# Performance work log

Hardware: AMD Instinct MI355X
Metric: run time of the kernel (lower is better)

The kernel has to match this reference:

```python
import jax, jax.numpy as jnp
import numpy as np
from itertools import combinations_with_replacement

LATENT_DIM = 16
N_PARAMS = 2
N_VARS = LATENT_DIM + N_PARAMS  # 18
POLY_ORDER = 3
BATCH = 131072

# Static exponent index tables: for each degree d, an [n_terms_d, d] array of
# variable indices (combinations with replacement), matching a sympy-style
# polynomial library [1, x_i, x_i*x_j, x_i*x_j*x_k, ...].
IDX = [np.array(list(combinations_with_replacement(range(N_VARS), d)), dtype=np.int32)
       for d in range(1, POLY_ORDER + 1)]
P = 1 + sum(a.shape[0] for a in IDX)  # 1330 library terms


def setup_inputs() -> dict:
    key = jax.random.key(0)
    k1, k2, k3 = jax.random.split(key, 3)
    z = jax.random.normal(k1, (BATCH, LATENT_DIM), dtype=jnp.float32)
    betas = jax.random.normal(k2, (BATCH, N_PARAMS), dtype=jnp.float32)
    big_xi = jax.random.normal(k3, (P, N_VARS), dtype=jnp.float32) * 0.1
    mask = jnp.ones((P, N_VARS), dtype=jnp.float32)
    return {"z": z, "betas": betas, "big_xi": big_xi, "mask": mask}


def _theta(x):
    # x: [B, N_VARS] -> theta: [B, P]
    cols = [jnp.ones((x.shape[0], 1), dtype=x.dtype)]  # constant term
    for idx in IDX:
        acc = x[:, idx[:, 0]]                # [B, n_terms_d]
        for k in range(1, idx.shape[1]):     # loop over degree (<= POLY_ORDER)
            acc = acc * x[:, idx[:, k]]
        cols.append(acc)
    return jnp.concatenate(cols, axis=1)


def reference(z, betas, big_xi, mask):
    x = jnp.concatenate([z, betas], axis=1)  # [B, N_VARS]
    theta = _theta(x)                        # [B, P]
    return theta @ (big_xi * mask)           # [B, N_VARS]
```

## Files before the change

kernel.cpp:

```cpp
#include <hip/hip_runtime.h>
#include <hip/hip_bf16.h>
#include <utility>


constexpr int NVARS   = 18;
constexpr int NOUT    = 18;
constexpr int NROWS   = 131072;
constexpr int PTERMS  = 1330;
constexpr int NSLOTS  = 672;
constexpr int NREPS   = 670;
constexpr int NCHUNKS = 84;

typedef __attribute__((ext_vector_type(8)))  short short8;
typedef __attribute__((ext_vector_type(16))) float f32x16;

struct T3 { int a, b, c; };

constexpr int sig(int v) { return v < 18 ? (v + 9) % 18 : v; }

constexpr T3 sigma3(T3 t) {
    int u0 = sig(t.a), u1 = sig(t.b), u2 = sig(t.c);
    int tmp = 0;
    if (u0 > u1) { tmp = u0; u0 = u1; u1 = tmp; }
    if (u1 > u2) { tmp = u1; u1 = u2; u2 = tmp; }
    if (u0 > u1) { tmp = u0; u0 = u1; u1 = tmp; }
    return T3{u0, u1, u2};
}

constexpr bool t3_less(T3 x, T3 y) {
    if (x.a != y.a) return x.a < y.a;
    if (x.b != y.b) return x.b < y.b;
    return x.c < y.c;
}
constexpr bool t3_eq(T3 x, T3 y) { return x.a == y.a && x.b == y.b && x.c == y.c; }

constexpr int rank_of(T3 t) {
    int deg = (t.a < 18) + (t.b < 18) + (t.c < 18);
    if (deg == 0) return 0;
    if (deg == 1) return 1 + t.a;
    if (deg == 2) {
        int r = 19;
        for (int a = 0; a < t.a; ++a) r += 18 - a;
        return r + (t.b - t.a);
    }
    int r = 190;
    for (int a = 0; a < t.a; ++a) { int n = 18 - a; r += n * (n + 1) / 2; }
    for (int b = t.a; b < t.b; ++b) r += 18 - b;
    return r + (t.c - t.b);
}

struct RepTables {
    signed char va[NSLOTS], vb[NSLOTS], vc[NSLOTS];
    short p0[NSLOTS], p1[NSLOTS];
};

constexpr RepTables make_tables() {
    RepTables R{};
    int s = 0;
    {
        T3 t{18, 18, 18};
        R.va[s] = 18; R.vb[s] = 18; R.vc[s] = 18;
        R.p0[s] = 0; R.p1[s] = -1;
        ++s;
    }
    for (int a = 0; a < NVARS; ++a) {
        T3 t{a, 18, 18};
        T3 st = sigma3(t);
        if (!t3_less(st, t)) {
            R.va[s] = (signed char)a; R.vb[s] = 18; R.vc[s] = 18;
            R.p0[s] = (short)rank_of(t);
            R.p1[s] = t3_eq(st, t) ? (short)-1 : (short)rank_of(st);
            ++s;
        }
    }
    for (int a = 0; a < NVARS; ++a)
        for (int b = a; b < NVARS; ++b) {
            T3 t{a, b, 18};
            T3 st = sigma3(t);
            if (!t3_less(st, t)) {
                R.va[s] = (signed char)a; R.vb[s] = (signed char)b; R.vc[s] = 18;
                R.p0[s] = (short)rank_of(t);
                R.p1[s] = t3_eq(st, t) ? (short)-1 : (short)rank_of(st);
                ++s;
            }
        }
    for (int a = 0; a < NVARS; ++a)
        for (int b = a; b < NVARS; ++b)
            for (int c = b; c < NVARS; ++c) {
                T3 t{a, b, c};
                T3 st = sigma3(t);
                if (!t3_less(st, t)) {
                    R.va[s] = (signed char)a; R.vb[s] = (signed char)b; R.vc[s] = (signed char)c;
                    R.p0[s] = (short)rank_of(t);
                    R.p1[s] = t3_eq(st, t) ? (short)-1 : (short)rank_of(st);
                    ++s;
                }
            }
    for (; s < NSLOTS; ++s) {
        R.va[s] = 19; R.vb[s] = 19; R.vc[s] = 19;
        R.p0[s] = -1; R.p1[s] = -1;
    }
    return R;
}

constexpr RepTables h_tab = make_tables();
__device__ const RepTables d_tab = make_tables();


__device__ __forceinline__ unsigned pack2(float f0, float f1) {
    unsigned u0 = __float_as_uint(f0) + 0x8000u;
    unsigned u1 = __float_as_uint(f1) + 0x8000u;
    return __builtin_amdgcn_perm(u1, u0, 0x07060302u);
}

template <int S>
__device__ __forceinline__ float term_val(const float (&x)[NVARS]) {
    constexpr int a = h_tab.va[S], b = h_tab.vb[S], c = h_tab.vc[S];
    if constexpr (a >= 19)      return 0.0f;
    else if constexpr (a == 18) return 1.0f;
    else if constexpr (b == 18) return x[a];
    else if constexpr (c == 18) return x[a] * x[b];
    else                        return x[a] * x[b] * x[c];
}

union AFrag { unsigned u[4]; short8 v; };

template <int CI, int... I>
__device__ __forceinline__ void eval8(const float (&x)[NVARS], float (&t)[8],
                                      std::integer_sequence<int, I...>) {
    ((t[I] = term_val<CI * 8 + I>(x)), ...);
}

template <int CI>
__device__ __forceinline__ void kstep(const float (&x)[NVARS],
                                      const short* __restrict__ wlane, f32x16& acc) {
    float t[8];
    eval8<CI>(x, t, std::make_integer_sequence<int, 8>{});
    AFrag af;
#pragma unroll
    for (int j = 0; j < 4; ++j) af.u[j] = pack2(t[2 * j], t[2 * j + 1]);
    short8 bf = *(const short8*)(wlane + CI * 512);
    acc = __builtin_amdgcn_mfma_f32_32x32x16_bf16(af.v, bf, acc, 0, 0, 0);
}

template <int... CI>
__device__ __forceinline__ void kloop(const float (&x)[NVARS],
                                      const short* __restrict__ wlane, f32x16& acc,
                                      std::integer_sequence<int, CI...>) {
    (kstep<CI>(x, wlane, acc), ...);
}

__global__ __launch_bounds__(256, 4) void vindy_mfma(const float* __restrict__ z,
                                                     const float* __restrict__ betas,
                                                     const short* __restrict__ wf,
                                                     float* __restrict__ out) {
    const int lane = threadIdx.x & 63;
    const int wave = threadIdx.x >> 6;
    const int m    = lane & 31;
    const int half = lane >> 5;
    const int row  = blockIdx.x * 128 + wave * 32 + m;

    float xr[NVARS];
    {
        const float4* z4 = (const float4*)(z + (size_t)row * 16);
        float4 v0 = z4[0], v1 = z4[1], v2 = z4[2], v3 = z4[3];
        xr[0]  = v0.x; xr[1]  = v0.y; xr[2]  = v0.z; xr[3]  = v0.w;
        xr[4]  = v1.x; xr[5]  = v1.y; xr[6]  = v1.z; xr[7]  = v1.w;
        xr[8]  = v2.x; xr[9]  = v2.y; xr[10] = v2.z; xr[11] = v2.w;
        xr[12] = v3.x; xr[13] = v3.y; xr[14] = v3.z; xr[15] = v3.w;
        const float2 b2 = *(const float2*)(betas + (size_t)row * 2);
        xr[16] = b2.x; xr[17] = b2.y;
    }
    const bool hp = (half != 0);
    float x[NVARS];
#pragma unroll
    for (int v = 0; v < NVARS; ++v) x[v] = hp ? xr[(v + 9) % NVARS] : xr[v];

    f32x16 acc;
#pragma unroll
    for (int i = 0; i < 16; ++i) acc[i] = 0.0f;

    const short* wlane = wf + lane * 8;
    kloop(x, wlane, acc, std::make_integer_sequence<int, NCHUNKS>{});

    if (m < NOUT) {
        float* op = out + ((size_t)(blockIdx.x * 128 + wave * 32 + half * 4)) * NOUT + m;
#pragma unroll
        for (int r = 0; r < 16; ++r) {
            int rr = (r & 3) + 8 * (r >> 2);
            op[(size_t)rr * NOUT] = acc[r];
        }
    }
}


__global__ void prep_wfrag(const float* __restrict__ xi, const float* __restrict__ mask,
                           __hip_bfloat16* __restrict__ wf) {
    int i = blockIdx.x * blockDim.x + threadIdx.x;
    if (i >= NCHUNKS * 64 * 8) return;
    int j = i & 7;
    int l = (i >> 3) & 63;
    int c = i >> 9;
    int s = c * 8 + j;
    int n = l & 31;
    int h = l >> 5;
    int p = h ? (int)d_tab.p1[s] : (int)d_tab.p0[s];
    float v = 0.0f;
    if (p >= 0 && n < NOUT) v = xi[p * NOUT + n] * mask[p * NOUT + n];
    wf[i] = __float2bfloat16(v);
}

extern "C" void kernel_launch(void* const* d_in, const int* in_sizes, int n_in,
                              void* d_out, int out_size, void* d_ws, size_t ws_size,
                              hipStream_t stream) {
    const float* z     = (const float*)d_in[0];
    const float* betas = (const float*)d_in[1];
    const float* xi    = (const float*)d_in[2];
    const float* mask  = (const float*)d_in[3];
    __hip_bfloat16* wf = (__hip_bfloat16*)d_ws;
    float* out = (float*)d_out;

    const int nprep = NCHUNKS * 64 * 8;
    prep_wfrag<<<(nprep + 255) / 256, 256, 0, stream>>>(xi, mask, wf);
    vindy_mfma<<<NROWS / 128, 256, 0, stream>>>(z, betas, (const short*)d_ws, out);
}
```

Before: 94.92 us.

## Use order-4 variable symmetry orbits with 16x16x32 MFMA to halve term evaluation

```diff
diff --git a/kernel.cpp b/kernel.cpp
--- a/kernel.cpp
+++ b/kernel.cpp
@@ -7,25 +7,30 @@
 constexpr int NOUT    = 18;
 constexpr int NROWS   = 131072;
 constexpr int PTERMS  = 1330;
-constexpr int NSLOTS  = 672;
-constexpr int NREPS   = 670;
-constexpr int NCHUNKS = 84;
-
-typedef __attribute__((ext_vector_type(8)))  short short8;
-typedef __attribute__((ext_vector_type(16))) float f32x16;
+constexpr int NCHUNKS = 43;
+constexpr int NSLOTS  = NCHUNKS * 8;
+
+typedef __attribute__((ext_vector_type(8))) short short8;
+typedef __attribute__((ext_vector_type(4))) float f32x4;
 
 struct T3 { int a, b, c; };
 
-constexpr int sig(int v) { return v < 18 ? (v + 9) % 18 : v; }
-
-constexpr T3 sigma3(T3 t) {
-    int u0 = sig(t.a), u1 = sig(t.b), u2 = sig(t.c);
-    int tmp = 0;
-    if (u0 > u1) { tmp = u0; u0 = u1; u1 = tmp; }
-    if (u1 > u2) { tmp = u1; u1 = u2; u2 = tmp; }
-    if (u0 > u1) { tmp = u0; u0 = u1; u1 = tmp; }
+constexpr int rho1(int v) {
+    if (v < 16)  return (v & ~3) | ((v + 1) & 3);
+    if (v == 16) return 17;
+    if (v == 17) return 16;
+    return v;
+}
+constexpr int rho2v(int v) { return rho1(rho1(v)); }
+
+constexpr T3 sort3(int u0, int u1, int u2) {
+    int t = 0;
+    if (u0 > u1) { t = u0; u0 = u1; u1 = t; }
+    if (u1 > u2) { t = u1; u1 = u2; u2 = t; }
+    if (u0 > u1) { t = u0; u0 = u1; u1 = t; }
     return T3{u0, u1, u2};
 }
+constexpr T3 rho3(T3 t) { return sort3(rho1(t.a), rho1(t.b), rho1(t.c)); }
 
 constexpr bool t3_less(T3 x, T3 y) {
     if (x.a != y.a) return x.a < y.a;
@@ -51,67 +56,64 @@
 
 struct RepTables {
     signed char va[NSLOTS], vb[NSLOTS], vc[NSLOTS];
-    short p0[NSLOTS], p1[NSLOTS];
+    short p[4][NSLOTS];
+    int count;
 };
+
+constexpr void consider(RepTables& R, int& s, T3 t) {
+    T3 im[4] = {t, T3{0, 0, 0}, T3{0, 0, 0}, T3{0, 0, 0}};
+    im[1] = rho3(im[0]);
+    im[2] = rho3(im[1]);
+    im[3] = rho3(im[2]);
+    for (int g = 1; g < 4; ++g)
+        if (t3_less(im[g], t)) return;
+    R.va[s] = (signed char)t.a; R.vb[s] = (signed char)t.b; R.vc[s] = (signed char)t.c;
+    for (int g = 0; g < 4; ++g) {
+        bool dup = false;
+        for (int h = 0; h < g; ++h)
+            if (t3_eq(im[h], im[g])) dup = true;
+        R.p[g][s] = dup ? (short)-1 : (short)rank_of(im[g]);
+    }
+    ++s;
+}
 
 constexpr RepTables make_tables() {
     RepTables R{};
     int s = 0;
-    {
-        T3 t{18, 18, 18};
-        R.va[s] = 18; R.vb[s] = 18; R.vc[s] = 18;
-        R.p0[s] = 0; R.p1[s] = -1;
-        ++s;
-    }
-    for (int a = 0; a < NVARS; ++a) {
-        T3 t{a, 18, 18};
-        T3 st = sigma3(t);
-        if (!t3_less(st, t)) {
-            R.va[s] = (signed char)a; R.vb[s] = 18; R.vc[s] = 18;
-            R.p0[s] = (short)rank_of(t);
-            R.p1[s] = t3_eq(st, t) ? (short)-1 : (short)rank_of(st);
-            ++s;
-        }
-    }
+    consider(R, s, T3{18, 18, 18});
+    for (int a = 0; a < NVARS; ++a) consider(R, s, T3{a, 18, 18});
     for (int a = 0; a < NVARS; ++a)
-        for (int b = a; b < NVARS; ++b) {
-            T3 t{a, b, 18};
-            T3 st = sigma3(t);
-            if (!t3_less(st, t)) {
-                R.va[s] = (signed char)a; R.vb[s] = (signed char)b; R.vc[s] = 18;
-                R.p0[s] = (short)rank_of(t);
-                R.p1[s] = t3_eq(st, t) ? (short)-1 : (short)rank_of(st);
-                ++s;
-            }
-        }
+        for (int b = a; b < NVARS; ++b) consider(R, s, T3{a, b, 18});
     for (int a = 0; a < NVARS; ++a)
         for (int b = a; b < NVARS; ++b)
-            for (int c = b; c < NVARS; ++c) {
-                T3 t{a, b, c};
-                T3 st = sigma3(t);
-                if (!t3_less(st, t)) {
-                    R.va[s] = (signed char)a; R.vb[s] = (signed char)b; R.vc[s] = (signed char)c;
-                    R.p0[s] = (short)rank_of(t);
-                    R.p1[s] = t3_eq(st, t) ? (short)-1 : (short)rank_of(st);
-                    ++s;
-                }
-            }
+            for (int c = b; c < NVARS; ++c) consider(R, s, T3{a, b, c});
+    R.count = s;
     for (; s < NSLOTS; ++s) {
         R.va[s] = 19; R.vb[s] = 19; R.vc[s] = 19;
-        R.p0[s] = -1; R.p1[s] = -1;
+        for (int g = 0; g < 4; ++g) R.p[g][s] = -1;
     }
     return R;
 }
 
 constexpr RepTables h_tab = make_tables();
+static_assert(h_tab.count == 342, "orbit enumeration must give 342 rep slots");
 __device__ const RepTables d_tab = make_tables();
 
 
+#if __has_builtin(__builtin_amdgcn_cvt_pk_bf16_f32)
+typedef __bf16 bf16x2 __attribute__((ext_vector_type(2)));
+__device__ __forceinline__ unsigned pack2(float f0, float f1) {
+    bf16x2 r = __builtin_amdgcn_cvt_pk_bf16_f32(f0, f1);
+    return __builtin_bit_cast(unsigned, r);
+}
+#else
 __device__ __forceinline__ unsigned pack2(float f0, float f1) {
     unsigned u0 = __float_as_uint(f0) + 0x8000u;
     unsigned u1 = __float_as_uint(f1) + 0x8000u;
     return __builtin_amdgcn_perm(u1, u0, 0x07060302u);
 }
+#endif
+
 
 template <int S>
 __device__ __forceinline__ float term_val(const float (&x)[NVARS]) {
@@ -133,63 +135,72 @@
 
 template <int CI>
 __device__ __forceinline__ void kstep(const float (&x)[NVARS],
-                                      const short* __restrict__ wlane, f32x16& acc) {
+                                      const short* __restrict__ wlane,
+                                      f32x4& acc0, f32x4& acc1) {
     float t[8];
     eval8<CI>(x, t, std::make_integer_sequence<int, 8>{});
     AFrag af;
 #pragma unroll
     for (int j = 0; j < 4; ++j) af.u[j] = pack2(t[2 * j], t[2 * j + 1]);
-    short8 bf = *(const short8*)(wlane + CI * 512);
-    acc = __builtin_amdgcn_mfma_f32_32x32x16_bf16(af.v, bf, acc, 0, 0, 0);
+    short8 b0 = *(const short8*)(wlane + (CI * 2 + 0) * 512);
+    short8 b1 = *(const short8*)(wlane + (CI * 2 + 1) * 512);
+    acc0 = __builtin_amdgcn_mfma_f32_16x16x32_bf16(af.v, b0, acc0, 0, 0, 0);
+    acc1 = __builtin_amdgcn_mfma_f32_16x16x32_bf16(af.v, b1, acc1, 0, 0, 0);
 }
 
 template <int... CI>
 __device__ __forceinline__ void kloop(const float (&x)[NVARS],
-                                      const short* __restrict__ wlane, f32x16& acc,
+                                      const short* __restrict__ wlane,
+                                      f32x4& acc0, f32x4& acc1,
                                       std::integer_sequence<int, CI...>) {
-    (kstep<CI>(x, wlane, acc), ...);
-}
-
-__global__ __launch_bounds__(256, 4) void vindy_mfma(const float* __restrict__ z,
+    (kstep<CI>(x, wlane, acc0, acc1), ...);
+}
+
+__global__ __launch_bounds__(256, 5) void vindy_mfma(const float* __restrict__ z,
                                                      const float* __restrict__ betas,
                                                      const short* __restrict__ wf,
                                                      float* __restrict__ out) {
     const int lane = threadIdx.x & 63;
     const int wave = threadIdx.x >> 6;
-    const int m    = lane & 31;
-    const int half = lane >> 5;
-    const int row  = blockIdx.x * 128 + wave * 32 + m;
-
-    float xr[NVARS];
+    const int g    = lane >> 4;
+    const int mcol = lane & 15;
+    const int rowbase = blockIdx.x * 64 + wave * 16;
+    const int arow = rowbase + mcol;
+
+    float x0[NVARS];
     {
-        const float4* z4 = (const float4*)(z + (size_t)row * 16);
+        const float4* z4 = (const float4*)(z + (size_t)arow * 16);
         float4 v0 = z4[0], v1 = z4[1], v2 = z4[2], v3 = z4[3];
-        xr[0]  = v0.x; xr[1]  = v0.y; xr[2]  = v0.z; xr[3]  = v0.w;
-        xr[4]  = v1.x; xr[5]  = v1.y; xr[6]  = v1.z; xr[7]  = v1.w;
-        xr[8]  = v2.x; xr[9]  = v2.y; xr[10] = v2.z; xr[11] = v2.w;
-        xr[12] = v3.x; xr[13] = v3.y; xr[14] = v3.z; xr[15] = v3.w;
-        const float2 b2 = *(const float2*)(betas + (size_t)row * 2);
-        xr[16] = b2.x; xr[17] = b2.y;
-    }
-    const bool hp = (half != 0);
-    float x[NVARS];
-#pragma unroll
-    for (int v = 0; v < NVARS; ++v) x[v] = hp ? xr[(v + 9) % NVARS] : xr[v];
-
-    f32x16 acc;
-#pragma unroll
-    for (int i = 0; i < 16; ++i) acc[i] = 0.0f;
+        x0[0]  = v0.x; x0[1]  = v0.y; x0[2]  = v0.z; x0[3]  = v0.w;
+        x0[4]  = v1.x; x0[5]  = v1.y; x0[6]  = v1.z; x0[7]  = v1.w;
+        x0[8]  = v2.x; x0[9]  = v2.y; x0[10] = v2.z; x0[11] = v2.w;
+        x0[12] = v3.x; x0[13] = v3.y; x0[14] = v3.z; x0[15] = v3.w;
+        const float2 b2 = *(const float2*)(betas + (size_t)arow * 2);
+        x0[16] = b2.x; x0[17] = b2.y;
+    }
+    const bool s1 = (g & 1) != 0;
+    const bool s2 = (g & 2) != 0;
+    float y[NVARS], x[NVARS];
+#pragma unroll
+    for (int v = 0; v < NVARS; ++v) y[v] = s1 ? x0[rho1(v)] : x0[v];
+#pragma unroll
+    for (int v = 0; v < NVARS; ++v) x[v] = s2 ? y[rho2v(v)] : y[v];
+
+    f32x4 acc0, acc1;
+#pragma unroll
+    for (int i = 0; i < 4; ++i) { acc0[i] = 0.0f; acc1[i] = 0.0f; }
 
     const short* wlane = wf + lane * 8;
-    kloop(x, wlane, acc, std::make_integer_sequence<int, NCHUNKS>{});
-
-    if (m < NOUT) {
-        float* op = out + ((size_t)(blockIdx.x * 128 + wave * 32 + half * 4)) * NOUT + m;
-#pragma unroll
-        for (int r = 0; r < 16; ++r) {
-            int rr = (r & 3) + 8 * (r >> 2);
-            op[(size_t)rr * NOUT] = acc[r];
-        }
+    kloop(x, wlane, acc0, acc1, std::make_integer_sequence<int, NCHUNKS>{});
+
+    const int orow = rowbase + g * 4;
+    float* op0 = out + (size_t)orow * NOUT + mcol;
+#pragma unroll
+    for (int r = 0; r < 4; ++r) op0[(size_t)r * NOUT] = acc0[r];
+    if (mcol < NOUT - 16) {
+        float* op1 = out + (size_t)orow * NOUT + 16 + mcol;
+#pragma unroll
+        for (int r = 0; r < 4; ++r) op1[(size_t)r * NOUT] = acc1[r];
     }
 }
 
@@ -197,14 +208,16 @@
 __global__ void prep_wfrag(const float* __restrict__ xi, const float* __restrict__ mask,
                            __hip_bfloat16* __restrict__ wf) {
     int i = blockIdx.x * blockDim.x + threadIdx.x;
-    if (i >= NCHUNKS * 64 * 8) return;
-    int j = i & 7;
-    int l = (i >> 3) & 63;
-    int c = i >> 9;
-    int s = c * 8 + j;
-    int n = l & 31;
-    int h = l >> 5;
-    int p = h ? (int)d_tab.p1[s] : (int)d_tab.p0[s];
+    if (i >= NCHUNKS * 2 * 64 * 8) return;
+    int j  = i & 7;
+    int l  = (i >> 3) & 63;
+    int ct = i >> 9;
+    int c  = ct >> 1;
+    int T  = ct & 1;
+    int gg = l >> 4;
+    int n  = T * 16 + (l & 15);
+    int s  = c * 8 + j;
+    int p  = (int)d_tab.p[gg][s];
     float v = 0.0f;
     if (p >= 0 && n < NOUT) v = xi[p * NOUT + n] * mask[p * NOUT + n];
     wf[i] = __float2bfloat16(v);
@@ -220,7 +233,7 @@
     __hip_bfloat16* wf = (__hip_bfloat16*)d_ws;
     float* out = (float*)d_out;
 
-    const int nprep = NCHUNKS * 64 * 8;
+    const int nprep = NCHUNKS * 2 * 64 * 8;
     prep_wfrag<<<(nprep + 255) / 256, 256, 0, stream>>>(xi, mask, wf);
-    vindy_mfma<<<NROWS / 128, 256, 0, stream>>>(z, betas, (const short*)d_ws, out);
-}
+    vindy_mfma<<<NROWS / 64, 256, 0, stream>>>(z, betas, (const short*)d_ws, out);
+}
```

Measured after the change: 92.82 us. -2.2%, faster.
